# Kernel optimization log

Measured on AMD Instinct MI355X. Metric: run time of the kernel, lower is better.

The kernel has to match this reference:

```python
import jax, jax.numpy as jnp
import numpy as np

E = 500_000   # edges
N = 100_000   # nodes
Q = 256       # queries
N_REL = 200
R = 2 * N_REL + 1  # relation table rows (401)
D = 64        # in_dim
A = 64        # attn_dim
O = 64        # out_dim


def setup_inputs() -> dict:
    key = jax.random.key(0)
    ks = jax.random.split(key, 16)
    s = 1.0 / np.sqrt(D)
    # edges columns: [query_idx, head_ent, rel, tail_ent, sub_node, obj_node]
    col_q = jax.random.randint(ks[0], (E, 1), 0, Q)
    col_h = jax.random.randint(ks[1], (E, 1), 0, N)
    col_r = jax.random.randint(ks[2], (E, 1), 0, R)
    col_t = jax.random.randint(ks[3], (E, 1), 0, N)
    col_s = jax.random.randint(ks[4], (E, 1), 0, N)
    col_o = jax.random.randint(ks[5], (E, 1), 0, N)
    edges = jnp.concatenate([col_q, col_h, col_r, col_t, col_s, col_o], axis=1)
    return {
        "q_sub": jax.random.randint(ks[6], (Q,), 0, N),
        "q_emb": jax.random.normal(ks[7], (Q, D), dtype=jnp.float32),
        "rela_embed": jax.random.normal(ks[8], (R, D), dtype=jnp.float32),
        "hidden": jax.random.normal(ks[9], (N, D), dtype=jnp.float32),
        "edges": edges,
        "n_nodes": N,
        "Ws_W": jax.random.normal(ks[10], (A, D), dtype=jnp.float32) * s,
        "Ws_b": jnp.zeros((A,), dtype=jnp.float32),
        "Wr_W": jax.random.normal(ks[11], (A, D), dtype=jnp.float32) * s,
        "Wq_W": jax.random.normal(ks[12], (A, D), dtype=jnp.float32) * s,
        "Wqr_W": jax.random.normal(ks[13], (A, D), dtype=jnp.float32) * s,
        "wa_W": jax.random.normal(ks[14], (1, A), dtype=jnp.float32) * s,
        "wa_b": jnp.zeros((1,), dtype=jnp.float32),
        "Wh_W": jax.random.normal(ks[15], (O, D), dtype=jnp.float32) * s,
    }


def reference(q_sub, q_emb, rela_embed, hidden, edges, n_nodes,
              Ws_W, Ws_b, Wr_W, Wq_W, Wqr_W, wa_W, wa_b, Wh_W):
    # sample_flag == 0 path of GNNLayer.forward (use_lama_rel == 1, act = identity)
    sub = edges[:, 4]
    rel = edges[:, 2]
    obj = edges[:, 5]
    hs = hidden[sub]            # [E, D] gather
    hr = rela_embed[rel]        # [E, D] gather
    h_qr = q_emb[edges[:, 0]]   # [E, D] gather
    # attention MLP: sigmoid(w_alpha(ReLU(Ws hs + Wr hr + Wq hqr + Wqr (hr*hqr))))
    pre = (jnp.einsum('ed,ad->ea', hs, Ws_W) + Ws_b
           + jnp.einsum('ed,ad->ea', hr, Wr_W)
           + jnp.einsum('ed,ad->ea', h_qr, Wq_W)
           + jnp.einsum('ed,ad->ea', hr * h_qr, Wqr_W))
    alpha = jax.nn.sigmoid(jnp.einsum('ea,oa->eo', jax.nn.relu(pre), wa_W) + wa_b)  # [E,1]
    message = alpha * (hs * hr)                                # [E, D]
    message_agg = jax.ops.segment_sum(message, obj, num_segments=n_nodes)  # [N, D] scatter-sum
    hidden_new = jnp.einsum('nd,od->no', message_agg, Wh_W)    # act = identity
    return hidden_new, alpha
```

## Files before the change

### kernel.cpp

```cpp
#include <hip/hip_runtime.h>
#include <hip/hip_bf16.h>

#define EDGES  500000
#define NNODES 100000
#define QN     256
#define RN     401
#define DD     64
#define AA     64
#define OO     64
#define XSB    1563
#define PB     1604

typedef __attribute__((ext_vector_type(8))) short short8;
typedef __attribute__((ext_vector_type(2))) short short2v;
typedef __attribute__((ext_vector_type(4))) float f32x4;
typedef __attribute__((ext_vector_type(2))) float f32x2;

__device__ inline unsigned short f2bf(float f) {
    union { float f; unsigned int u; } v; v.f = f;
    unsigned int u = v.u;
    u += 0x7FFFu + ((u >> 16) & 1u);
    return (unsigned short)(u >> 16);
}

__device__ inline f32x2 bfpair2f(unsigned int u) {
    union { unsigned int i; float f; } lo, hi;
    lo.i = u << 16;
    hi.i = u & 0xFFFF0000u;
    f32x2 r; r[0] = lo.f; r[1] = hi.f; return r;
}

__device__ inline short8 load8_cvt(const float* __restrict__ p) {
    f32x4 x0 = ((const f32x4*)p)[0];
    f32x4 x1 = ((const f32x4*)p)[1];
    short8 r;
    r[0] = (short)f2bf(x0[0]); r[1] = (short)f2bf(x0[1]);
    r[2] = (short)f2bf(x0[2]); r[3] = (short)f2bf(x0[3]);
    r[4] = (short)f2bf(x1[0]); r[5] = (short)f2bf(x1[1]);
    r[6] = (short)f2bf(x1[2]); r[7] = (short)f2bf(x1[3]);
    return r;
}

__device__ inline short8 load8_cvt_prod(const float* __restrict__ pa,
                                        const float* __restrict__ pb) {
    f32x4 a0 = ((const f32x4*)pa)[0];
    f32x4 a1 = ((const f32x4*)pa)[1];
    f32x4 b0 = ((const f32x4*)pb)[0];
    f32x4 b1 = ((const f32x4*)pb)[1];
    short8 r;
    r[0] = (short)f2bf(a0[0]*b0[0]); r[1] = (short)f2bf(a0[1]*b0[1]);
    r[2] = (short)f2bf(a0[2]*b0[2]); r[3] = (short)f2bf(a0[3]*b0[3]);
    r[4] = (short)f2bf(a1[0]*b1[0]); r[5] = (short)f2bf(a1[1]*b1[1]);
    r[6] = (short)f2bf(a1[2]*b1[2]); r[7] = (short)f2bf(a1[3]*b1[3]);
    return r;
}

__device__ inline void atomic_pk_add_bf16(short* addr, short2v v) {
#if __has_builtin(__builtin_amdgcn_global_atomic_fadd_v2bf16)
    __builtin_amdgcn_global_atomic_fadd_v2bf16(
        (__attribute__((address_space(1))) short2v*)addr, v);
#else
    asm volatile("global_atomic_pk_add_bf16 %0, %1, off"
                 :: "v"(addr), "v"(v) : "memory");
#endif
}

__global__ void k_pre(const float* __restrict__ hidden,
                      const float* __restrict__ Ws_W,
                      const float* __restrict__ q_emb,
                      const float* __restrict__ rela,
                      const float* __restrict__ Wq_W,
                      const float* __restrict__ Wr_W,
                      const float* __restrict__ Wqr_W,
                      const float* __restrict__ Ws_b,
                      short* __restrict__ Xs,
                      short* __restrict__ hidden_bf,
                      short* __restrict__ P,
                      short* __restrict__ agg) {
    __shared__ short W[AA * 200];
    int tid = threadIdx.x;
    int wave = tid >> 6, lane = tid & 63;
    int quad = lane >> 4, l15 = lane & 15;

    if (blockIdx.x < XSB) {
        int rowbase_blk = blockIdx.x * 64;
        {
            const short8 z = short8{0,0,0,0,0,0,0,0};
            int base = rowbase_blk * DD + tid * 16;
            int row0 = rowbase_blk + (tid * 16) / DD;
            if (row0 < NNODES) {
                *(short8*)(agg + base) = z;
                *(short8*)(agg + base + 8) = z;
            }
        }
        for (int idx = tid; idx < AA * DD; idx += 256) {
            int a = idx >> 6, d = idx & 63;
            W[a * 72 + d] = (short)f2bf(Ws_W[idx]);
        }
        __syncthreads();
        int rowbase = rowbase_blk + wave * 16;
        int row_a = rowbase + l15;

        f32x4 acc[4];
        for (int t = 0; t < 4; ++t) { acc[t][0]=acc[t][1]=acc[t][2]=acc[t][3]=0.f; }

#pragma unroll
        for (int ks = 0; ks < 2; ++ks) {
            int ka = ks * 32 + quad * 8;
            short8 afrag;
            if (row_a < NNODES) {
                afrag = load8_cvt(hidden + (size_t)row_a * DD + ka);
                *(short8*)(hidden_bf + (size_t)row_a * DD + ka) = afrag;
            } else {
                afrag = short8{0,0,0,0,0,0,0,0};
            }
#pragma unroll
            for (int t = 0; t < 4; ++t) {
                short8 bfrag = *(const short8*)&W[(t * 16 + l15) * 72 + ka];
                acc[t] = __builtin_amdgcn_mfma_f32_16x16x32_bf16(afrag, bfrag, acc[t], 0, 0, 0);
            }
        }
#pragma unroll
        for (int t = 0; t < 4; ++t)
#pragma unroll
            for (int r = 0; r < 4; ++r) {
                int row = rowbase + quad * 4 + r;
                if (row < NNODES) Xs[(size_t)row * AA + t * 16 + l15] = (short)f2bf(acc[t][r]);
            }
    } else {
        int pb = blockIdx.x - XSB;
        for (int idx = tid; idx < AA * 192; idx += 256) {
            int a = idx / 192, k = idx - a * 192;
            float v = (k < 64) ? Wq_W[a * 64 + k]
                    : (k < 128) ? Wr_W[a * 64 + (k - 64)]
                                : Wqr_W[a * 64 + (k - 128)];
            W[a * 200 + k] = (short)f2bf(v);
        }
        __syncthreads();
        int pairbase = pb * 64 + wave * 16;
        int mypair = pairbase + l15;
        int q = mypair / RN;
        int r = mypair - q * RN;
        const float* hq = q_emb + (size_t)q * DD;
        const float* hr = rela  + (size_t)r * DD;

        f32x4 acc[4];
#pragma unroll
        for (int t = 0; t < 4; ++t) {
            float b = Ws_b[t * 16 + l15];
            acc[t][0] = acc[t][1] = acc[t][2] = acc[t][3] = b;
        }

#pragma unroll
        for (int ks = 0; ks < 6; ++ks) {
            int ka = ks * 32 + quad * 8;
            short8 afrag;
            if (ka < 64)       afrag = load8_cvt(hq + ka);
            else if (ka < 128) afrag = load8_cvt(hr + (ka - 64));
            else               afrag = load8_cvt_prod(hq + (ka - 128), hr + (ka - 128));
#pragma unroll
            for (int t = 0; t < 4; ++t) {
                short8 bfrag = *(const short8*)&W[(t * 16 + l15) * 200 + ka];
                acc[t] = __builtin_amdgcn_mfma_f32_16x16x32_bf16(afrag, bfrag, acc[t], 0, 0, 0);
            }
        }
#pragma unroll
        for (int t = 0; t < 4; ++t)
#pragma unroll
            for (int rg = 0; rg < 4; ++rg) {
                int row = pairbase + quad * 4 + rg;
                P[(size_t)row * AA + t * 16 + l15] = (short)f2bf(acc[t][rg]);
            }
    }
}

__global__ void k_edge(const int* __restrict__ edges,
                       const short* __restrict__ Xs,
                       const short* __restrict__ P,
                       const short* __restrict__ hidden_bf,
                       const float* __restrict__ rela,
                       const float* __restrict__ wa_W,
                       const float* __restrict__ wa_b,
                       short* __restrict__ agg,
                       float* __restrict__ alpha_out) {
    int tid  = threadIdx.x;
    int wave = tid >> 6, lane = tid & 63;
    int l32  = lane & 31;
    int half = lane >> 5;
    size_t e = (size_t)blockIdx.x * 8 + wave * 2 + half;

    const int* ep = edges + e * 6;
    int q = ep[0];
    int r = ep[2];
    int2 so = *(const int2*)&ep[4];
    int sub = so.x, obj = so.y;

    int c2 = 2 * l32;
    unsigned int xs_u = *(const unsigned int*)&Xs[(size_t)sub * AA + c2];
    unsigned int pp_u = *(const unsigned int*)&P[((size_t)q * RN + r) * AA + c2];
    f32x2 xs = bfpair2f(xs_u);
    f32x2 pp = bfpair2f(pp_u);
    f32x2 wa = *(const f32x2*)&wa_W[c2];

    float v = fmaxf(xs[0] + pp[0], 0.f) * wa[0]
            + fmaxf(xs[1] + pp[1], 0.f) * wa[1];
#pragma unroll
    for (int off = 16; off > 0; off >>= 1) v += __shfl_xor(v, off, 64);
    float alpha = 1.f / (1.f + __expf(-(v + wa_b[0])));
    if (l32 == 0) alpha_out[e] = alpha;

    unsigned int hs_u = *(const unsigned int*)&hidden_bf[(size_t)sub * DD + c2];
    f32x2 hs = bfpair2f(hs_u);
    f32x2 hr = *(const f32x2*)&rela[(size_t)r * DD + c2];
    short2v m;
    m[0] = (short)f2bf(alpha * hs[0] * hr[0]);
    m[1] = (short)f2bf(alpha * hs[1] * hr[1]);
    atomic_pk_add_bf16((short*)agg + (size_t)obj * DD + c2, m);
}

__global__ void k_out(const short* __restrict__ agg,
                      const float* __restrict__ Wh_W,
                      float* __restrict__ out) {
    __shared__ short W[OO * 72];
    int tid = threadIdx.x;
    for (int idx = tid; idx < OO * DD; idx += 256) {
        int o = idx >> 6, d = idx & 63;
        W[o * 72 + d] = (short)f2bf(Wh_W[idx]);
    }
    __syncthreads();
    int wave = tid >> 6, lane = tid & 63;
    int quad = lane >> 4, l15 = lane & 15;
    int rowbase = blockIdx.x * 64 + wave * 16;
    int row_a = rowbase + l15;

    f32x4 acc[4];
    for (int t = 0; t < 4; ++t) { acc[t][0]=acc[t][1]=acc[t][2]=acc[t][3]=0.f; }

#pragma unroll
    for (int ks = 0; ks < 2; ++ks) {
        int ka = ks * 32 + quad * 8;
        short8 afrag;
        if (row_a < NNODES) afrag = *(const short8*)(agg + (size_t)row_a * DD + ka);
        else                afrag = short8{0,0,0,0,0,0,0,0};
#pragma unroll
        for (int t = 0; t < 4; ++t) {
            short8 bfrag = *(const short8*)&W[(t * 16 + l15) * 72 + ka];
            acc[t] = __builtin_amdgcn_mfma_f32_16x16x32_bf16(afrag, bfrag, acc[t], 0, 0, 0);
        }
    }
#pragma unroll
    for (int t = 0; t < 4; ++t)
#pragma unroll
        for (int r = 0; r < 4; ++r) {
            int row = rowbase + quad * 4 + r;
            if (row < NNODES) out[(size_t)row * OO + t * 16 + l15] = acc[t][r];
        }
}

extern "C" void kernel_launch(void* const* d_in, const int* in_sizes, int n_in,
                              void* d_out, int out_size, void* d_ws, size_t ws_size,
                              hipStream_t stream) {
    const float* q_emb  = (const float*)d_in[1];
    const float* rela   = (const float*)d_in[2];
    const float* hidden = (const float*)d_in[3];
    const int*   edges  = (const int*)d_in[4];
    const float* Ws_W   = (const float*)d_in[6];
    const float* Ws_b   = (const float*)d_in[7];
    const float* Wr_W   = (const float*)d_in[8];
    const float* Wq_W   = (const float*)d_in[9];
    const float* Wqr_W  = (const float*)d_in[10];
    const float* wa_W   = (const float*)d_in[11];
    const float* wa_b   = (const float*)d_in[12];
    const float* Wh_W   = (const float*)d_in[13];

    short* Xs        = (short*)d_ws;
    short* P         = Xs + (size_t)NNODES * AA;
    short* hidden_bf = P + (size_t)QN * RN * AA;
    short* agg       = hidden_bf + (size_t)NNODES * DD;

    float* out       = (float*)d_out;
    float* alpha_out = out + (size_t)NNODES * OO;

    k_pre<<<XSB + PB, 256, 0, stream>>>(hidden, Ws_W, q_emb, rela,
                                        Wq_W, Wr_W, Wqr_W, Ws_b,
                                        Xs, hidden_bf, P, agg);
    k_edge<<<EDGES / 8, 256, 0, stream>>>(edges, Xs, P, hidden_bf, rela, wa_W, wa_b,
                                          agg, alpha_out);
    k_out<<<(NNODES + 63) / 64, 256, 0, stream>>>(agg, Wh_W, out);
}
```

Baseline: 205.2 us.

## Fuse three kernels into one persistent cooperative kernel with grid syncs

Replaces the three launches (precompute, edge scatter, output projection) with a single persistent cooperative kernel whose blocks grid-stride over each phase, separated by grid-wide syncs. The edge phase also handles two edge groups per iteration so more gathers are in flight. This targets launch gaps and tail effects between kernels. In exchange it caps resident blocks, which can lower latency hiding in the gather/atomic-heavy edge phase, and adds the cost of two grid barriers. The separate kernels stay as a fallback when cooperative launch is unavailable.

```diff
diff --git a/kernel.cpp b/kernel.cpp
--- a/kernel.cpp
+++ b/kernel.cpp
@@ -1,5 +1,6 @@
 #include <hip/hip_runtime.h>
 #include <hip/hip_bf16.h>
+#include <hip/hip_cooperative_groups.h>
 
 #define EDGES  500000
 #define NNODES 100000
@@ -10,6 +11,7 @@
 #define OO     64
 #define XSB    1563
 #define PB     1604
+#define EVB    62500
 
 typedef __attribute__((ext_vector_type(8))) short short8;
 typedef __attribute__((ext_vector_type(2))) short short2v;
@@ -65,58 +67,54 @@
 #endif
 }
 
-__global__ void k_pre(const float* __restrict__ hidden,
-                      const float* __restrict__ Ws_W,
-                      const float* __restrict__ q_emb,
-                      const float* __restrict__ rela,
-                      const float* __restrict__ Wq_W,
-                      const float* __restrict__ Wr_W,
-                      const float* __restrict__ Wqr_W,
-                      const float* __restrict__ Ws_b,
-                      short* __restrict__ Xs,
-                      short* __restrict__ hidden_bf,
-                      short* __restrict__ P,
-                      short* __restrict__ agg) {
-    __shared__ short W[AA * 200];
-    int tid = threadIdx.x;
-    int wave = tid >> 6, lane = tid & 63;
-    int quad = lane >> 4, l15 = lane & 15;
-
-    if (blockIdx.x < XSB) {
-        int rowbase_blk = blockIdx.x * 64;
+struct Params {
+    const float* hidden; const float* Ws_W; const float* q_emb; const float* rela;
+    const float* Wq_W;   const float* Wr_W; const float* Wqr_W; const float* Ws_b;
+    const int*   edges;  const float* wa_W; const float* wa_b;  const float* Wh_W;
+    short* Xs; short* hidden_bf; short* P; short* agg;
+    float* out; float* alpha_out;
+};
+
+__global__ void __launch_bounds__(256, 4) mega(Params pr) {
+    __shared__ short smem[AA * 200];
+    const int tid  = threadIdx.x;
+    const int wave = tid >> 6, lane = tid & 63;
+    const int quad = lane >> 4, l15 = lane & 15;
+    const int G = gridDim.x;
+
+    for (int idx = tid; idx < AA * DD; idx += 256) {
+        int a = idx >> 6, d = idx & 63;
+        smem[a * 72 + d] = (short)f2bf(pr.Ws_W[idx]);
+    }
+    __syncthreads();
+    for (int vb = blockIdx.x; vb < XSB; vb += G) {
+        int rowbase_blk = vb * 64;
         {
             const short8 z = short8{0,0,0,0,0,0,0,0};
             int base = rowbase_blk * DD + tid * 16;
-            int row0 = rowbase_blk + (tid * 16) / DD;
+            int row0 = rowbase_blk + (tid >> 2);
             if (row0 < NNODES) {
-                *(short8*)(agg + base) = z;
-                *(short8*)(agg + base + 8) = z;
-            }
-        }
-        for (int idx = tid; idx < AA * DD; idx += 256) {
-            int a = idx >> 6, d = idx & 63;
-            W[a * 72 + d] = (short)f2bf(Ws_W[idx]);
-        }
-        __syncthreads();
+                *(short8*)(pr.agg + base) = z;
+                *(short8*)(pr.agg + base + 8) = z;
+            }
+        }
         int rowbase = rowbase_blk + wave * 16;
         int row_a = rowbase + l15;
-
         f32x4 acc[4];
         for (int t = 0; t < 4; ++t) { acc[t][0]=acc[t][1]=acc[t][2]=acc[t][3]=0.f; }
-
 #pragma unroll
         for (int ks = 0; ks < 2; ++ks) {
             int ka = ks * 32 + quad * 8;
             short8 afrag;
             if (row_a < NNODES) {
-                afrag = load8_cvt(hidden + (size_t)row_a * DD + ka);
-                *(short8*)(hidden_bf + (size_t)row_a * DD + ka) = afrag;
+                afrag = load8_cvt(pr.hidden + (size_t)row_a * DD + ka);
+                *(short8*)(pr.hidden_bf + (size_t)row_a * DD + ka) = afrag;
             } else {
                 afrag = short8{0,0,0,0,0,0,0,0};
             }
 #pragma unroll
             for (int t = 0; t < 4; ++t) {
-                short8 bfrag = *(const short8*)&W[(t * 16 + l15) * 72 + ka];
+                short8 bfrag = *(const short8*)&smem[(t * 16 + l15) * 72 + ka];
                 acc[t] = __builtin_amdgcn_mfma_f32_16x16x32_bf16(afrag, bfrag, acc[t], 0, 0, 0);
             }
         }
@@ -125,32 +123,33 @@
 #pragma unroll
             for (int r = 0; r < 4; ++r) {
                 int row = rowbase + quad * 4 + r;
-                if (row < NNODES) Xs[(size_t)row * AA + t * 16 + l15] = (short)f2bf(acc[t][r]);
-            }
-    } else {
-        int pb = blockIdx.x - XSB;
-        for (int idx = tid; idx < AA * 192; idx += 256) {
-            int a = idx / 192, k = idx - a * 192;
-            float v = (k < 64) ? Wq_W[a * 64 + k]
-                    : (k < 128) ? Wr_W[a * 64 + (k - 64)]
-                                : Wqr_W[a * 64 + (k - 128)];
-            W[a * 200 + k] = (short)f2bf(v);
-        }
-        __syncthreads();
-        int pairbase = pb * 64 + wave * 16;
+                if (row < NNODES)
+                    pr.Xs[(size_t)row * AA + t * 16 + l15] = (short)f2bf(acc[t][r]);
+            }
+    }
+    __syncthreads();
+
+    for (int idx = tid; idx < AA * 192; idx += 256) {
+        int a = idx / 192, k = idx - a * 192;
+        float v = (k < 64) ? pr.Wq_W[a * 64 + k]
+                : (k < 128) ? pr.Wr_W[a * 64 + (k - 64)]
+                            : pr.Wqr_W[a * 64 + (k - 128)];
+        smem[a * 200 + k] = (short)f2bf(v);
+    }
+    __syncthreads();
+    for (int vb = blockIdx.x; vb < PB; vb += G) {
+        int pairbase = vb * 64 + wave * 16;
         int mypair = pairbase + l15;
         int q = mypair / RN;
         int r = mypair - q * RN;
-        const float* hq = q_emb + (size_t)q * DD;
-        const float* hr = rela  + (size_t)r * DD;
-
+        const float* hq = pr.q_emb + (size_t)q * DD;
+        const float* hr = pr.rela  + (size_t)r * DD;
         f32x4 acc[4];
 #pragma unroll
         for (int t = 0; t < 4; ++t) {
-            float b = Ws_b[t * 16 + l15];
+            float b = pr.Ws_b[t * 16 + l15];
             acc[t][0] = acc[t][1] = acc[t][2] = acc[t][3] = b;
         }
-
 #pragma unroll
         for (int ks = 0; ks < 6; ++ks) {
             int ka = ks * 32 + quad * 8;
@@ -160,6 +159,195 @@
             else               afrag = load8_cvt_prod(hq + (ka - 128), hr + (ka - 128));
 #pragma unroll
             for (int t = 0; t < 4; ++t) {
+                short8 bfrag = *(const short8*)&smem[(t * 16 + l15) * 200 + ka];
+                acc[t] = __builtin_amdgcn_mfma_f32_16x16x32_bf16(afrag, bfrag, acc[t], 0, 0, 0);
+            }
+        }
+#pragma unroll
+        for (int t = 0; t < 4; ++t)
+#pragma unroll
+            for (int rg = 0; rg < 4; ++rg) {
+                int row = pairbase + quad * 4 + rg;
+                pr.P[(size_t)row * AA + t * 16 + l15] = (short)f2bf(acc[t][rg]);
+            }
+    }
+
+    __threadfence();
+    cooperative_groups::this_grid().sync();
+
+    {
+        const int l32 = lane & 31;
+        const int half = lane >> 5;
+        const int c2 = 2 * l32;
+        const f32x2 wa = *(const f32x2*)&pr.wa_W[c2];
+        const float wab = pr.wa_b[0];
+        for (int vb = blockIdx.x; vb < EVB; vb += 2 * G) {
+            int vbB = vb + G;
+            bool hasB = vbB < EVB;
+            size_t eA = (size_t)vb * 8 + wave * 2 + half;
+            size_t eB = (size_t)(hasB ? vbB : vb) * 8 + wave * 2 + half;
+            const int* epA = pr.edges + eA * 6;
+            const int* epB = pr.edges + eB * 6;
+            int qA = epA[0], rA = epA[2];
+            int2 soA = *(const int2*)&epA[4];
+            int qB = epB[0], rB = epB[2];
+            int2 soB = *(const int2*)&epB[4];
+            unsigned xsA = *(const unsigned*)&pr.Xs[(size_t)soA.x * AA + c2];
+            unsigned ppA = *(const unsigned*)&pr.P[((size_t)qA * RN + rA) * AA + c2];
+            unsigned hsA = *(const unsigned*)&pr.hidden_bf[(size_t)soA.x * DD + c2];
+            f32x2 hrA = *(const f32x2*)&pr.rela[(size_t)rA * DD + c2];
+            unsigned xsB = *(const unsigned*)&pr.Xs[(size_t)soB.x * AA + c2];
+            unsigned ppB = *(const unsigned*)&pr.P[((size_t)qB * RN + rB) * AA + c2];
+            unsigned hsB = *(const unsigned*)&pr.hidden_bf[(size_t)soB.x * DD + c2];
+            f32x2 hrB = *(const f32x2*)&pr.rela[(size_t)rB * DD + c2];
+            {
+                f32x2 xs = bfpair2f(xsA), pp = bfpair2f(ppA);
+                float v = fmaxf(xs[0] + pp[0], 0.f) * wa[0]
+                        + fmaxf(xs[1] + pp[1], 0.f) * wa[1];
+#pragma unroll
+                for (int off = 16; off > 0; off >>= 1) v += __shfl_xor(v, off, 64);
+                float alpha = 1.f / (1.f + __expf(-(v + wab)));
+                if (l32 == 0) pr.alpha_out[eA] = alpha;
+                f32x2 hs = bfpair2f(hsA);
+                short2v m;
+                m[0] = (short)f2bf(alpha * hs[0] * hrA[0]);
+                m[1] = (short)f2bf(alpha * hs[1] * hrA[1]);
+                atomic_pk_add_bf16(pr.agg + (size_t)soA.y * DD + c2, m);
+            }
+            if (hasB) {
+                f32x2 xs = bfpair2f(xsB), pp = bfpair2f(ppB);
+                float v = fmaxf(xs[0] + pp[0], 0.f) * wa[0]
+                        + fmaxf(xs[1] + pp[1], 0.f) * wa[1];
+#pragma unroll
+                for (int off = 16; off > 0; off >>= 1) v += __shfl_xor(v, off, 64);
+                float alpha = 1.f / (1.f + __expf(-(v + wab)));
+                if (l32 == 0) pr.alpha_out[eB] = alpha;
+                f32x2 hs = bfpair2f(hsB);
+                short2v m;
+                m[0] = (short)f2bf(alpha * hs[0] * hrB[0]);
+                m[1] = (short)f2bf(alpha * hs[1] * hrB[1]);
+                atomic_pk_add_bf16(pr.agg + (size_t)soB.y * DD + c2, m);
+            }
+        }
+    }
+
+    __threadfence();
+    cooperative_groups::this_grid().sync();
+
+    __syncthreads();
+    for (int idx = tid; idx < OO * DD; idx += 256) {
+        int o = idx >> 6, d = idx & 63;
+        smem[o * 72 + d] = (short)f2bf(pr.Wh_W[idx]);
+    }
+    __syncthreads();
+    for (int vb = blockIdx.x; vb < XSB; vb += G) {
+        int rowbase = vb * 64 + wave * 16;
+        int row_a = rowbase + l15;
+        f32x4 acc[4];
+        for (int t = 0; t < 4; ++t) { acc[t][0]=acc[t][1]=acc[t][2]=acc[t][3]=0.f; }
+#pragma unroll
+        for (int ks = 0; ks < 2; ++ks) {
+            int ka = ks * 32 + quad * 8;
+            short8 afrag;
+            if (row_a < NNODES) afrag = *(const short8*)(pr.agg + (size_t)row_a * DD + ka);
+            else                afrag = short8{0,0,0,0,0,0,0,0};
+#pragma unroll
+            for (int t = 0; t < 4; ++t) {
+                short8 bfrag = *(const short8*)&smem[(t * 16 + l15) * 72 + ka];
+                acc[t] = __builtin_amdgcn_mfma_f32_16x16x32_bf16(afrag, bfrag, acc[t], 0, 0, 0);
+            }
+        }
+#pragma unroll
+        for (int t = 0; t < 4; ++t)
+#pragma unroll
+            for (int r = 0; r < 4; ++r) {
+                int row = rowbase + quad * 4 + r;
+                if (row < NNODES) pr.out[(size_t)row * OO + t * 16 + l15] = acc[t][r];
+            }
+    }
+}
+
+__global__ void k_pre(Params pr) {
+    __shared__ short W[AA * 200];
+    int tid = threadIdx.x;
+    int wave = tid >> 6, lane = tid & 63;
+    int quad = lane >> 4, l15 = lane & 15;
+
+    if (blockIdx.x < XSB) {
+        int rowbase_blk = blockIdx.x * 64;
+        {
+            const short8 z = short8{0,0,0,0,0,0,0,0};
+            int base = rowbase_blk * DD + tid * 16;
+            int row0 = rowbase_blk + (tid >> 2);
+            if (row0 < NNODES) {
+                *(short8*)(pr.agg + base) = z;
+                *(short8*)(pr.agg + base + 8) = z;
+            }
+        }
+        for (int idx = tid; idx < AA * DD; idx += 256) {
+            int a = idx >> 6, d = idx & 63;
+            W[a * 72 + d] = (short)f2bf(pr.Ws_W[idx]);
+        }
+        __syncthreads();
+        int rowbase = rowbase_blk + wave * 16;
+        int row_a = rowbase + l15;
+        f32x4 acc[4];
+        for (int t = 0; t < 4; ++t) { acc[t][0]=acc[t][1]=acc[t][2]=acc[t][3]=0.f; }
+#pragma unroll
+        for (int ks = 0; ks < 2; ++ks) {
+            int ka = ks * 32 + quad * 8;
+            short8 afrag;
+            if (row_a < NNODES) {
+                afrag = load8_cvt(pr.hidden + (size_t)row_a * DD + ka);
+                *(short8*)(pr.hidden_bf + (size_t)row_a * DD + ka) = afrag;
+            } else {
+                afrag = short8{0,0,0,0,0,0,0,0};
+            }
+#pragma unroll
+            for (int t = 0; t < 4; ++t) {
+                short8 bfrag = *(const short8*)&W[(t * 16 + l15) * 72 + ka];
+                acc[t] = __builtin_amdgcn_mfma_f32_16x16x32_bf16(afrag, bfrag, acc[t], 0, 0, 0);
+            }
+        }
+#pragma unroll
+        for (int t = 0; t < 4; ++t)
+#pragma unroll
+            for (int r = 0; r < 4; ++r) {
+                int row = rowbase + quad * 4 + r;
+                if (row < NNODES)
+                    pr.Xs[(size_t)row * AA + t * 16 + l15] = (short)f2bf(acc[t][r]);
+            }
+    } else {
+        int pb = blockIdx.x - XSB;
+        for (int idx = tid; idx < AA * 192; idx += 256) {
+            int a = idx / 192, k = idx - a * 192;
+            float v = (k < 64) ? pr.Wq_W[a * 64 + k]
+                    : (k < 128) ? pr.Wr_W[a * 64 + (k - 64)]
+                                : pr.Wqr_W[a * 64 + (k - 128)];
+            W[a * 200 + k] = (short)f2bf(v);
+        }
+        __syncthreads();
+        int pairbase = pb * 64 + wave * 16;
+        int mypair = pairbase + l15;
+        int q = mypair / RN;
+        int r = mypair - q * RN;
+        const float* hq = pr.q_emb + (size_t)q * DD;
+        const float* hr = pr.rela  + (size_t)r * DD;
+        f32x4 acc[4];
+#pragma unroll
+        for (int t = 0; t < 4; ++t) {
+            float b = pr.Ws_b[t * 16 + l15];
+            acc[t][0] = acc[t][1] = acc[t][2] = acc[t][3] = b;
+        }
+#pragma unroll
+        for (int ks = 0; ks < 6; ++ks) {
+            int ka = ks * 32 + quad * 8;
+            short8 afrag;
+            if (ka < 64)       afrag = load8_cvt(hq + ka);
+            else if (ka < 128) afrag = load8_cvt(hr + (ka - 64));
+            else               afrag = load8_cvt_prod(hq + (ka - 128), hr + (ka - 128));
+#pragma unroll
+            for (int t = 0; t < 4; ++t) {
                 short8 bfrag = *(const short8*)&W[(t * 16 + l15) * 200 + ka];
                 acc[t] = __builtin_amdgcn_mfma_f32_16x16x32_bf16(afrag, bfrag, acc[t], 0, 0, 0);
             }
@@ -169,78 +357,66 @@
 #pragma unroll
             for (int rg = 0; rg < 4; ++rg) {
                 int row = pairbase + quad * 4 + rg;
-                P[(size_t)row * AA + t * 16 + l15] = (short)f2bf(acc[t][rg]);
-            }
-    }
-}
-
-__global__ void k_edge(const int* __restrict__ edges,
-                       const short* __restrict__ Xs,
-                       const short* __restrict__ P,
-                       const short* __restrict__ hidden_bf,
-                       const float* __restrict__ rela,
-                       const float* __restrict__ wa_W,
-                       const float* __restrict__ wa_b,
-                       short* __restrict__ agg,
-                       float* __restrict__ alpha_out) {
+                pr.P[(size_t)row * AA + t * 16 + l15] = (short)f2bf(acc[t][rg]);
+            }
+    }
+}
+
+__global__ void k_edge(Params pr) {
     int tid  = threadIdx.x;
     int wave = tid >> 6, lane = tid & 63;
     int l32  = lane & 31;
     int half = lane >> 5;
     size_t e = (size_t)blockIdx.x * 8 + wave * 2 + half;
 
-    const int* ep = edges + e * 6;
+    const int* ep = pr.edges + e * 6;
     int q = ep[0];
     int r = ep[2];
     int2 so = *(const int2*)&ep[4];
     int sub = so.x, obj = so.y;
 
     int c2 = 2 * l32;
-    unsigned int xs_u = *(const unsigned int*)&Xs[(size_t)sub * AA + c2];
-    unsigned int pp_u = *(const unsigned int*)&P[((size_t)q * RN + r) * AA + c2];
+    unsigned xs_u = *(const unsigned*)&pr.Xs[(size_t)sub * AA + c2];
+    unsigned pp_u = *(const unsigned*)&pr.P[((size_t)q * RN + r) * AA + c2];
     f32x2 xs = bfpair2f(xs_u);
     f32x2 pp = bfpair2f(pp_u);
-    f32x2 wa = *(const f32x2*)&wa_W[c2];
+    f32x2 wa = *(const f32x2*)&pr.wa_W[c2];
 
     float v = fmaxf(xs[0] + pp[0], 0.f) * wa[0]
             + fmaxf(xs[1] + pp[1], 0.f) * wa[1];
 #pragma unroll
     for (int off = 16; off > 0; off >>= 1) v += __shfl_xor(v, off, 64);
-    float alpha = 1.f / (1.f + __expf(-(v + wa_b[0])));
-    if (l32 == 0) alpha_out[e] = alpha;
-
-    unsigned int hs_u = *(const unsigned int*)&hidden_bf[(size_t)sub * DD + c2];
+    float alpha = 1.f / (1.f + __expf(-(v + pr.wa_b[0])));
+    if (l32 == 0) pr.alpha_out[e] = alpha;
+
+    unsigned hs_u = *(const unsigned*)&pr.hidden_bf[(size_t)sub * DD + c2];
     f32x2 hs = bfpair2f(hs_u);
-    f32x2 hr = *(const f32x2*)&rela[(size_t)r * DD + c2];
+    f32x2 hr = *(const f32x2*)&pr.rela[(size_t)r * DD + c2];
     short2v m;
     m[0] = (short)f2bf(alpha * hs[0] * hr[0]);
     m[1] = (short)f2bf(alpha * hs[1] * hr[1]);
-    atomic_pk_add_bf16((short*)agg + (size_t)obj * DD + c2, m);
-}
-
-__global__ void k_out(const short* __restrict__ agg,
-                      const float* __restrict__ Wh_W,
-                      float* __restrict__ out) {
+    atomic_pk_add_bf16(pr.agg + (size_t)obj * DD + c2, m);
+}
+
+__global__ void k_out(Params pr) {
     __shared__ short W[OO * 72];
     int tid = threadIdx.x;
     for (int idx = tid; idx < OO * DD; idx += 256) {
         int o = idx >> 6, d = idx & 63;
-        W[o * 72 + d] = (short)f2bf(Wh_W[idx]);
+        W[o * 72 + d] = (short)f2bf(pr.Wh_W[idx]);
     }
     __syncthreads();
     int wave = tid >> 6, lane = tid & 63;
     int quad = lane >> 4, l15 = lane & 15;
     int rowbase = blockIdx.x * 64 + wave * 16;
     int row_a = rowbase + l15;
-
     f32x4 acc[4];
     for (int t = 0; t < 4; ++t) { acc[t][0]=acc[t][1]=acc[t][2]=acc[t][3]=0.f; }
-
 #pragma unroll
     for (int ks = 0; ks < 2; ++ks) {
         int ka = ks * 32 + quad * 8;
         short8 afrag;
-        if (row_a < NNODES) afrag = *(const short8*)(agg + (size_t)row_a * DD + ka);
+        if (row_a < NNODES) afrag = *(const short8*)(pr.agg + (size_t)row_a * DD + ka);
         else                afrag = short8{0,0,0,0,0,0,0,0};
 #pragma unroll
         for (int t = 0; t < 4; ++t) {
@@ -253,38 +429,54 @@
 #pragma unroll
         for (int r = 0; r < 4; ++r) {
             int row = rowbase + quad * 4 + r;
-            if (row < NNODES) out[(size_t)row * OO + t * 16 + l15] = acc[t][r];
+            if (row < NNODES) pr.out[(size_t)row * OO + t * 16 + l15] = acc[t][r];
         }
 }
 
 extern "C" void kernel_launch(void* const* d_in, const int* in_sizes, int n_in,
                               void* d_out, int out_size, void* d_ws, size_t ws_size,
                               hipStream_t stream) {
-    const float* q_emb  = (const float*)d_in[1];
-    const float* rela   = (const float*)d_in[2];
-    const float* hidden = (const float*)d_in[3];
-    const int*   edges  = (const int*)d_in[4];
-    const float* Ws_W   = (const float*)d_in[6];
-    const float* Ws_b   = (const float*)d_in[7];
-    const float* Wr_W   = (const float*)d_in[8];
-    const float* Wq_W   = (const float*)d_in[9];
-    const float* Wqr_W  = (const float*)d_in[10];
-    const float* wa_W   = (const float*)d_in[11];
-    const float* wa_b   = (const float*)d_in[12];
-    const float* Wh_W   = (const float*)d_in[13];
+    Params pr;
+    pr.q_emb  = (const float*)d_in[1];
+    pr.rela   = (const float*)d_in[2];
+    pr.hidden = (const float*)d_in[3];
+    pr.edges  = (const int*)d_in[4];
+    pr.Ws_W   = (const float*)d_in[6];
+    pr.Ws_b   = (const float*)d_in[7];
+    pr.Wr_W   = (const float*)d_in[8];
+    pr.Wq_W   = (const float*)d_in[9];
+    pr.Wqr_W  = (const float*)d_in[10];
+    pr.wa_W   = (const float*)d_in[11];
+    pr.wa_b   = (const float*)d_in[12];
+    pr.Wh_W   = (const float*)d_in[13];
 
     short* Xs        = (short*)d_ws;
     short* P         = Xs + (size_t)NNODES * AA;
     short* hidden_bf = P + (size_t)QN * RN * AA;
     short* agg       = hidden_bf + (size_t)NNODES * DD;
-
-    float* out       = (float*)d_out;
-    float* alpha_out = out + (size_t)NNODES * OO;
-
-    k_pre<<<XSB + PB, 256, 0, stream>>>(hidden, Ws_W, q_emb, rela,
-                                        Wq_W, Wr_W, Wqr_W, Ws_b,
-                                        Xs, hidden_bf, P, agg);
-    k_edge<<<EDGES / 8, 256, 0, stream>>>(edges, Xs, P, hidden_bf, rela, wa_W, wa_b,
-                                          agg, alpha_out);
-    k_out<<<(NNODES + 63) / 64, 256, 0, stream>>>(agg, Wh_W, out);
-}
+    pr.Xs = Xs; pr.P = P; pr.hidden_bf = hidden_bf; pr.agg = agg;
+
+    pr.out       = (float*)d_out;
+    pr.alpha_out = pr.out + (size_t)NNODES * OO;
+
+    hipError_t err = hipErrorUnknown;
+    int dev = 0;
+    if (hipGetDevice(&dev) == hipSuccess) {
+        int coop = 0, nCU = 0, perCU = 0;
+        (void)hipDeviceGetAttribute(&coop, hipDeviceAttributeCooperativeLaunch, dev);
+        (void)hipDeviceGetAttribute(&nCU, hipDeviceAttributeMultiprocessorCount, dev);
+        (void)hipOccupancyMaxActiveBlocksPerMultiprocessor(&perCU, mega, 256, 0);
+        if (coop && nCU > 0 && perCU > 0) {
+            int grid = perCU * nCU;
+            if (grid > 2048) grid = 2048;
+            void* args[] = { &pr };
+            err = hipLaunchCooperativeKernel((const void*)mega, dim3(grid), dim3(256),
+                                             args, 0, stream);
+        }
+    }
+    if (err != hipSuccess) {
+        k_pre<<<XSB + PB, 256, 0, stream>>>(pr);
+        k_edge<<<EVB, 256, 0, stream>>>(pr);
+        k_out<<<XSB, 256, 0, stream>>>(pr);
+    }
+}
```

New measurement: 510.0 us. +148.6%, slower.
